# Kernel optimization log

Hardware: AMD Instinct MI355X
Metric: run time of the kernel (lower is better)

The kernel has to match this reference:

```python
import jax, jax.numpy as jnp
import numpy as np

N_AGENTS, BATCH, SEQ, HID = 256, 64, 20, 128
RADIUS = 0.15


def setup_inputs() -> dict:
    key = jax.random.key(0)
    k1, k2 = jax.random.split(key)
    agent_hidden_states = jax.random.normal(k1, (N_AGENTS, BATCH, SEQ, HID), dtype=jnp.float32)
    agent_positions = jax.random.uniform(k2, (N_AGENTS, BATCH, SEQ, 2), dtype=jnp.float32)
    radius = jnp.float32(RADIUS)
    return {"agent_hidden_states": agent_hidden_states,
            "agent_positions": agent_positions,
            "radius": radius}


def reference(agent_hidden_states, agent_positions, radius):
    # pool_type == 'mean': for each target agent i, average the last-step hidden
    # states of all other agents j whose last-step position is within `radius`.
    h_last = agent_hidden_states[:, :, -1, :]      # [N, B, H]
    p_last = agent_positions[:, :, -1, :]          # [N, B, 2]
    N = h_last.shape[0]
    # pairwise last-step distances: [N_target, N_neighbor, B]
    diff = p_last[:, None, :, :] - p_last[None, :, :, :]
    dist = jnp.sqrt(jnp.sum(diff * diff, axis=-1))
    within = (dist <= radius) & (~jnp.eye(N, dtype=bool))[:, :, None]  # exclude self
    m = within.astype(h_last.dtype)                # [N, N, B]
    # masked sum of neighbor hiddens, divided by neighbor count (clamped to 1)
    ctx_sum = jnp.einsum('ijb,jbh->ibh', m, h_last)       # [N, B, H]
    count = jnp.clip(jnp.sum(m, axis=1), 1.0)             # [N, B]
    return ctx_sum / count[..., None]
```

## Files before the change

kernel.cpp:

```cpp
#include <hip/hip_runtime.h>

constexpr int NA = 256;
constexpr int B  = 64;
constexpr int S  = 20;
constexpr int H  = 128;

__global__ __launch_bounds__(128, 4) void social_pool_kernel(
    const float* __restrict__ h,
    const float* __restrict__ p,
    const float* __restrict__ rptr,
    float* __restrict__ out)
{
    const int i   = blockIdx.x & (NA - 1);
    const int b   = blockIdx.x >> 8;
    const int tid = threadIdx.x;

    __shared__ float px[NA];
    __shared__ float py[NA];
    __shared__ int   nbr[NA];
    __shared__ int   cnt;
    if (tid == 0) cnt = 0;

    for (int j = tid; j < NA; j += 128) {
        const float2 pj = *(const float2*)(p + (((size_t)(j * B + b)) * S + (S - 1)) * 2);
        px[j] = pj.x;
        py[j] = pj.y;
    }
    __syncthreads();

    const float r  = *rptr;
    const float xi = px[i];
    const float yi = py[i];

    for (int j = tid; j < NA; j += 128) {
        const float dx   = __fsub_rn(xi, px[j]);
        const float dy   = __fsub_rn(yi, py[j]);
        const float d2   = __fadd_rn(__fmul_rn(dx, dx), __fmul_rn(dy, dy));
        const float dist = __fsqrt_rn(d2);
        if (dist <= r && j != i) {
            const int k = atomicAdd(&cnt, 1);
            nbr[k] = j;
        }
    }
    __syncthreads();
    const int n = cnt;

    float acc = 0.0f;
    const size_t hbase = ((size_t)b * S + (S - 1)) * H + tid;
    const size_t jstride = (size_t)B * S * H;
    for (int k = 0; k < n; ++k) {
        const int j = nbr[k];
        acc += h[(size_t)j * jstride + hbase];
    }

    const float c = (float)(n > 0 ? n : 1);
    out[((size_t)i * B + b) * H + tid] = __fdiv_rn(acc, c);
}

extern "C" void kernel_launch(void* const* d_in, const int* in_sizes, int n_in,
                              void* d_out, int out_size, void* d_ws, size_t ws_size,
                              hipStream_t stream) {
    const float* h    = (const float*)d_in[0];
    const float* p    = (const float*)d_in[1];
    const float* rptr = (const float*)d_in[2];
    float* out        = (float*)d_out;

    (void)in_sizes; (void)n_in; (void)out_size; (void)d_ws; (void)ws_size;

    social_pool_kernel<<<dim3(NA * B), dim3(128), 0, stream>>>(h, p, rptr, out);
}
```

Baseline: 231.6 us.

## Process 16 agents per block with wave ballots and float2 neighbor gathers

Each 256-thread block now handles 16 target agents for one batch, with one wave per four targets. Neighbor masks are built with wave ballots instead of shared atomics and a shared neighbor list, so the shared-memory barriers go away and the position tile loaded per block is reused across targets. Each lane gathers float2 hidden values, and four independent loads are issued per iteration from the four mask words to raise memory-level parallelism. The risk is that sequential per-agent loops inside a wave reduce parallelism, and the accumulation order changes slightly.

```diff
diff --git a/kernel.cpp b/kernel.cpp
--- a/kernel.cpp
+++ b/kernel.cpp
@@ -5,56 +5,81 @@
 constexpr int S  = 20;
 constexpr int H  = 128;
 
-__global__ __launch_bounds__(128, 4) void social_pool_kernel(
+constexpr int AGENTS_PER_BLOCK = 16;
+constexpr int BLOCKS = (NA / AGENTS_PER_BLOCK) * B;
+
+__global__ __launch_bounds__(256, 4) void social_pool_kernel(
     const float* __restrict__ h,
     const float* __restrict__ p,
     const float* __restrict__ rptr,
     float* __restrict__ out)
 {
-    const int i   = blockIdx.x & (NA - 1);
-    const int b   = blockIdx.x >> 8;
-    const int tid = threadIdx.x;
+    const int group = blockIdx.x & (NA / AGENTS_PER_BLOCK - 1);
+    const int b     = blockIdx.x >> 4;
+    const int tid   = threadIdx.x;
+    const int wave  = tid >> 6;
+    const int lane  = tid & 63;
 
     __shared__ float px[NA];
     __shared__ float py[NA];
-    __shared__ int   nbr[NA];
-    __shared__ int   cnt;
-    if (tid == 0) cnt = 0;
 
-    for (int j = tid; j < NA; j += 128) {
+    {
+        const int j = tid;
         const float2 pj = *(const float2*)(p + (((size_t)(j * B + b)) * S + (S - 1)) * 2);
         px[j] = pj.x;
         py[j] = pj.y;
     }
     __syncthreads();
 
-    const float r  = *rptr;
-    const float xi = px[i];
-    const float yi = py[i];
+    const float r = *rptr;
 
-    for (int j = tid; j < NA; j += 128) {
-        const float dx   = __fsub_rn(xi, px[j]);
-        const float dy   = __fsub_rn(yi, py[j]);
-        const float d2   = __fadd_rn(__fmul_rn(dx, dx), __fmul_rn(dy, dy));
-        const float dist = __fsqrt_rn(d2);
-        if (dist <= r && j != i) {
-            const int k = atomicAdd(&cnt, 1);
-            nbr[k] = j;
+    const size_t jstride = (size_t)B * S * H;
+    const float* hb = h + ((size_t)b * S + (S - 1)) * H + 2 * lane;
+
+    for (int a = 0; a < 4; ++a) {
+        const int i = group * AGENTS_PER_BLOCK + wave * 4 + a;
+        const float xi = px[i];
+        const float yi = py[i];
+
+        unsigned long long m[4];
+        #pragma unroll
+        for (int k = 0; k < 4; ++k) {
+            const int j = (k << 6) + lane;
+            const float dx   = __fsub_rn(xi, px[j]);
+            const float dy   = __fsub_rn(yi, py[j]);
+            const float d2   = __fadd_rn(__fmul_rn(dx, dx), __fmul_rn(dy, dy));
+            const float dist = __fsqrt_rn(d2);
+            m[k] = __ballot(dist <= r);
         }
+        m[i >> 6] &= ~(1ull << (i & 63));
+
+        const int n = __popcll(m[0]) + __popcll(m[1]) + __popcll(m[2]) + __popcll(m[3]);
+
+        float ax = 0.0f, ay = 0.0f;
+        while (m[0] | m[1] | m[2] | m[3]) {
+            float2 v[4];
+            bool got[4];
+            #pragma unroll
+            for (int k = 0; k < 4; ++k) {
+                got[k] = (m[k] != 0ull);
+                if (got[k]) {
+                    const int j = (k << 6) + __builtin_ctzll(m[k]);
+                    m[k] &= m[k] - 1ull;
+                    v[k] = *(const float2*)(hb + (size_t)j * jstride);
+                }
+            }
+            #pragma unroll
+            for (int k = 0; k < 4; ++k) {
+                if (got[k]) { ax += v[k].x; ay += v[k].y; }
+            }
+        }
+
+        const float c = (float)(n > 0 ? n : 1);
+        float2 o;
+        o.x = __fdiv_rn(ax, c);
+        o.y = __fdiv_rn(ay, c);
+        *(float2*)(out + ((size_t)i * B + b) * H + 2 * lane) = o;
     }
-    __syncthreads();
-    const int n = cnt;
-
-    float acc = 0.0f;
-    const size_t hbase = ((size_t)b * S + (S - 1)) * H + tid;
-    const size_t jstride = (size_t)B * S * H;
-    for (int k = 0; k < n; ++k) {
-        const int j = nbr[k];
-        acc += h[(size_t)j * jstride + hbase];
-    }
-
-    const float c = (float)(n > 0 ? n : 1);
-    out[((size_t)i * B + b) * H + tid] = __fdiv_rn(acc, c);
 }
 
 extern "C" void kernel_launch(void* const* d_in, const int* in_sizes, int n_in,
@@ -67,5 +92,5 @@
 
     (void)in_sizes; (void)n_in; (void)out_size; (void)d_ws; (void)ws_size;
 
-    social_pool_kernel<<<dim3(NA * B), dim3(128), 0, stream>>>(h, p, rptr, out);
+    social_pool_kernel<<<dim3(BLOCKS), dim3(256), 0, stream>>>(h, p, rptr, out);
 }
```

Measured after the change: 217.1 us. -6.3%, faster.
